# Kernel tuning notes

Hardware: AMD Instinct MI355X
Metric: run time of the kernel (lower is better)

Reference implementation:

```python
import jax, jax.numpy as jnp
import numpy as np

N_NEIGHBORS = 16
N_CLASSES = 10

def setup_inputs() -> dict:
    key = jax.random.key(0)
    k1, k2, k3 = jax.random.split(key, 3)
    x = jax.random.normal(k1, (1024, 64), dtype=jnp.float32)
    train_data = jax.random.normal(k2, (100000, 64), dtype=jnp.float32)
    train_labels = jax.random.randint(k3, (100000,), 0, N_CLASSES, dtype=jnp.int64)
    return {"x": x, "train_data": train_data, "train_labels": train_labels}

def reference(x, train_data, train_labels):
    # Pairwise L2 distances [B, N] via the quadratic expansion (same math as cdist p=2)
    x2 = jnp.sum(x * x, axis=-1, keepdims=True)            # [B, 1]
    t2 = jnp.sum(train_data * train_data, axis=-1)          # [N]
    d2 = x2 - 2.0 * (x @ train_data.T) + t2                 # [B, N]
    dist = jnp.sqrt(jnp.maximum(d2, 0.0))
    # k smallest distances
    neg_d, idx = jax.lax.top_k(-dist, N_NEIGHBORS)           # [B, k]
    d = -neg_d
    labels = train_labels[idx]                               # [B, k] gather
    # weights = 'distance': inverse distance, with exact-match rows handled
    w = 1.0 / d
    inf_mask = jnp.isinf(w)
    inf_row = jnp.any(inf_mask, axis=1, keepdims=True)
    w = jnp.where(inf_row, inf_mask.astype(w.dtype), w)
    # scatter_add weighted votes into [B, C]
    B = x.shape[0]
    rows = jnp.arange(B)[:, None]
    proba = jnp.zeros((B, N_CLASSES), dtype=w.dtype).at[rows, labels].add(w)
    s = jnp.sum(proba, axis=1, keepdims=True)
    s = jnp.where(s == 0.0, jnp.float32(1.0), s)
    proba = proba / s
    return jnp.argmax(proba, axis=1), proba
```

## Files before the change

### kernel.cpp

```cpp
#include <hip/hip_runtime.h>
#include <math.h>


constexpr int D        = 64;
constexpr int K        = 16;
constexpr int NCLS     = 10;
constexpr int CHUNKLEN = 896;
constexpr int NCHUNK   = 112;
constexpr int NPAD     = NCHUNK * CHUNKLEN + 32;
constexpr int NSUB     = 64;
constexpr int SUBLEN   = 128;
constexpr int SLOT     = 16;
constexpr int MSEL     = 48;

typedef __attribute__((ext_vector_type(8))) short bf16x8_t;
typedef __attribute__((ext_vector_type(4))) float f32x4_t;
typedef unsigned short ushort_t;

__device__ __forceinline__ ushort_t f32_to_bf16_rne(float f) {
  unsigned int u = __float_as_uint(f);
  unsigned int r = u + 0x7FFFu + ((u >> 16) & 1u);
  return (ushort_t)(r >> 16);
}

__device__ __forceinline__ bf16x8_t pack_bf16x8(float4 a, float4 b) {
  union { ushort_t u[8]; bf16x8_t v; } r;
  r.u[0] = f32_to_bf16_rne(a.x); r.u[1] = f32_to_bf16_rne(a.y);
  r.u[2] = f32_to_bf16_rne(a.z); r.u[3] = f32_to_bf16_rne(a.w);
  r.u[4] = f32_to_bf16_rne(b.x); r.u[5] = f32_to_bf16_rne(b.y);
  r.u[6] = f32_to_bf16_rne(b.z); r.u[7] = f32_to_bf16_rne(b.w);
  return r.v;
}

__global__ __launch_bounds__(256) void cvt_train(
    const float* __restrict__ t, ushort_t* __restrict__ tb,
    float* __restrict__ t2, float* __restrict__ nt2h, int N)
{
  int gid = blockIdx.x * 256 + threadIdx.x;
  int row = gid >> 2, qt = gid & 3;
  if (row >= NPAD) return;
  ushort_t* dst = tb + (size_t)row * D + qt * 16;
  if (row >= N) {
    uint2 z = make_uint2(0u, 0u);
    #pragma unroll
    for (int i = 0; i < 4; ++i) *reinterpret_cast<uint2*>(dst + i * 4) = z;
    if (qt == 0) { t2[row] = INFINITY; nt2h[row] = -INFINITY; }
    return;
  }
  const float* src = t + (size_t)row * D + qt * 16;
  float nrm = 0.f;
  #pragma unroll
  for (int i = 0; i < 4; ++i) {
    float4 v = *reinterpret_cast<const float4*>(src + i * 4);
    nrm = fmaf(v.x, v.x, nrm); nrm = fmaf(v.y, v.y, nrm);
    nrm = fmaf(v.z, v.z, nrm); nrm = fmaf(v.w, v.w, nrm);
    uint2 hh = make_uint2(
      (unsigned)f32_to_bf16_rne(v.x) | ((unsigned)f32_to_bf16_rne(v.y) << 16),
      (unsigned)f32_to_bf16_rne(v.z) | ((unsigned)f32_to_bf16_rne(v.w) << 16));
    *reinterpret_cast<uint2*>(dst + i * 4) = hh;
  }
  nrm += __shfl_xor(nrm, 1);
  nrm += __shfl_xor(nrm, 2);
  if (qt == 0) { t2[row] = nrm; nt2h[row] = -0.5f * nrm; }
}

__global__ __launch_bounds__(256) void knn_sample(
    const ushort_t* __restrict__ tb, const float* __restrict__ x,
    const float* __restrict__ nt2h, float* __restrict__ samp)
{
  const int tid = threadIdx.x;
  const int w = tid >> 6, lane = tid & 63;
  const int lh = lane & 15, lg = lane >> 4;
  const int qb = blockIdx.x, sub = blockIdx.y;
  const int q = qb * 64 + w * 16 + lh;

  const float* xrp = x + (size_t)q * D + lg * 8;
  bf16x8_t B0 = pack_bf16x8(*reinterpret_cast<const float4*>(xrp),
                            *reinterpret_cast<const float4*>(xrp + 4));
  bf16x8_t B1 = pack_bf16x8(*reinterpret_cast<const float4*>(xrp + 32),
                            *reinterpret_cast<const float4*>(xrp + 36));

  float Ld[4] = {-INFINITY, -INFINITY, -INFINITY, -INFINITY};

  const int pstart = sub * SUBLEN;
  const ushort_t* abase = tb + (size_t)pstart * D + lh * D + lg * 8;
  const float* nbase = nt2h + pstart + lg * 4;

  bf16x8_t A0[4], A1[4]; float4 NH[4];
  #pragma unroll
  for (int j = 0; j < 4; ++j) {
    const ushort_t* ap = abase + (size_t)j * 16 * D;
    A0[j] = *reinterpret_cast<const bf16x8_t*>(ap);
    A1[j] = *reinterpret_cast<const bf16x8_t*>(ap + 32);
    NH[j] = *reinterpret_cast<const float4*>(nbase + j * 16);
  }
  bf16x8_t N0[4], N1[4]; float4 NN[4];
  #pragma unroll
  for (int j = 0; j < 4; ++j) {
    const ushort_t* ap = abase + (size_t)(4 + j) * 16 * D;
    N0[j] = *reinterpret_cast<const bf16x8_t*>(ap);
    N1[j] = *reinterpret_cast<const bf16x8_t*>(ap + 32);
    NN[j] = *reinterpret_cast<const float4*>(nbase + (4 + j) * 16);
  }

  #pragma unroll
  for (int j = 0; j < 4; ++j) {
    f32x4_t c = {NH[j].x, NH[j].y, NH[j].z, NH[j].w};
    c = __builtin_amdgcn_mfma_f32_16x16x32_bf16(A0[j], B0, c, 0, 0, 0);
    c = __builtin_amdgcn_mfma_f32_16x16x32_bf16(A1[j], B1, c, 0, 0, 0);
    #pragma unroll
    for (int r = 0; r < 4; ++r) {
      float sv = c[r];
      if (sv > Ld[3]) {
        Ld[3] = sv;
        if (Ld[3] > Ld[2]) { float s_ = Ld[3]; Ld[3] = Ld[2]; Ld[2] = s_; }
        if (Ld[2] > Ld[1]) { float s_ = Ld[2]; Ld[2] = Ld[1]; Ld[1] = s_; }
        if (Ld[1] > Ld[0]) { float s_ = Ld[1]; Ld[1] = Ld[0]; Ld[0] = s_; }
      }
    }
  }
  #pragma unroll
  for (int j = 0; j < 4; ++j) {
    f32x4_t c = {NN[j].x, NN[j].y, NN[j].z, NN[j].w};
    c = __builtin_amdgcn_mfma_f32_16x16x32_bf16(N0[j], B0, c, 0, 0, 0);
    c = __builtin_amdgcn_mfma_f32_16x16x32_bf16(N1[j], B1, c, 0, 0, 0);
    #pragma unroll
    for (int r = 0; r < 4; ++r) {
      float sv = c[r];
      if (sv > Ld[3]) {
        Ld[3] = sv;
        if (Ld[3] > Ld[2]) { float s_ = Ld[3]; Ld[3] = Ld[2]; Ld[2] = s_; }
        if (Ld[2] > Ld[1]) { float s_ = Ld[2]; Ld[2] = Ld[1]; Ld[1] = s_; }
        if (Ld[1] > Ld[0]) { float s_ = Ld[1]; Ld[1] = Ld[0]; Ld[0] = s_; }
      }
    }
  }

  float* outp = samp + (size_t)q * (NSUB * 16) + sub * 16 + lg * 4;
  *reinterpret_cast<float4*>(outp) = make_float4(Ld[0], Ld[1], Ld[2], Ld[3]);
}

__global__ __launch_bounds__(256) void knn_theta(
    const float* __restrict__ samp, float* __restrict__ theta, int B)
{
  const int w = threadIdx.x >> 6, lane = threadIdx.x & 63;
  const int q = blockIdx.x * 4 + w;
  if (q >= B) return;

  const float* s = samp + (size_t)q * (NSUB * 16) + lane * 16;
  float4 p0 = *reinterpret_cast<const float4*>(s);
  float4 p1 = *reinterpret_cast<const float4*>(s + 4);
  float4 p2 = *reinterpret_cast<const float4*>(s + 8);
  float4 p3 = *reinterpret_cast<const float4*>(s + 12);
  float L0[4] = {p0.x, p0.y, p0.z, p0.w};
  float L1[4] = {p1.x, p1.y, p1.z, p1.w};
  float L2[4] = {p2.x, p2.y, p2.z, p2.w};
  float L3[4] = {p3.x, p3.y, p3.z, p3.w};

  float th = -INFINITY;
  for (int r = 0; r < K; ++r) {
    float bd = fmaxf(fmaxf(L0[0], L1[0]), fmaxf(L2[0], L3[0]));
    #pragma unroll
    for (int sdx = 0; sdx < 6; ++sdx) bd = fmaxf(bd, __shfl_xor(bd, 32 >> sdx));
    if (L0[0] == bd) { L0[0] = L0[1]; L0[1] = L0[2]; L0[2] = L0[3]; L0[3] = -INFINITY; }
    if (L1[0] == bd) { L1[0] = L1[1]; L1[1] = L1[2]; L1[2] = L1[3]; L1[3] = -INFINITY; }
    if (L2[0] == bd) { L2[0] = L2[1]; L2[1] = L2[2]; L2[2] = L2[3]; L2[3] = -INFINITY; }
    if (L3[0] == bd) { L3[0] = L3[1]; L3[1] = L3[2]; L3[2] = L3[3]; L3[3] = -INFINITY; }
    th = bd;
  }
  if (lane == 0) theta[q] = th;
}

__global__ __launch_bounds__(256) void knn_filter(
    const ushort_t* __restrict__ tb, const float* __restrict__ x,
    const float* __restrict__ nt2h, const float* __restrict__ theta,
    int* __restrict__ cnts, int2* __restrict__ cand2)
{
  __shared__ int  cnt_l[64];
  __shared__ int2 list_p[64][SLOT];

  const int tid = threadIdx.x;
  const int w = tid >> 6, lane = tid & 63;
  const int lh = lane & 15, lg = lane >> 4;

  const int d   = blockIdx.x + 16 * blockIdx.y;
  const int xcd = d & 7;
  const int t_  = d >> 3;
  const int qb  = t_ & 15;
  const int ch  = ((t_ >> 4) << 3) | xcd;

  const int q0 = qb * 64;
  const int wp0 = ch * CHUNKLEN + w * (CHUNKLEN / 4);

  if (tid < 64) cnt_l[tid] = 0;
  __syncthreads();

  bf16x8_t Bq0[4], Bq1[4];
  float th[4];
  #pragma unroll
  for (int ct = 0; ct < 4; ++ct) {
    const float* xrp = x + (size_t)(q0 + ct * 16 + lh) * D + lg * 8;
    Bq0[ct] = pack_bf16x8(*reinterpret_cast<const float4*>(xrp),
                          *reinterpret_cast<const float4*>(xrp + 4));
    Bq1[ct] = pack_bf16x8(*reinterpret_cast<const float4*>(xrp + 32),
                          *reinterpret_cast<const float4*>(xrp + 36));
    th[ct] = theta[q0 + ct * 16 + lh];
  }

  const ushort_t* abase = tb + (size_t)wp0 * D + lh * D + lg * 8;
  const float* nbase = nt2h + wp0 + lg * 4;

  bf16x8_t cA0 = *reinterpret_cast<const bf16x8_t*>(abase);
  bf16x8_t cA1 = *reinterpret_cast<const bf16x8_t*>(abase + 32);
  float4   cNA = *reinterpret_cast<const float4*>(nbase);
  bf16x8_t cB0 = *reinterpret_cast<const bf16x8_t*>(abase + (size_t)16 * D);
  bf16x8_t cB1 = *reinterpret_cast<const bf16x8_t*>(abase + (size_t)16 * D + 32);
  float4   cNB = *reinterpret_cast<const float4*>(nbase + 16);

  #define PROCESS(A0_, A1_, NH_, GIDX_)                                           \
    {                                                                             \
      _Pragma("unroll")                                                           \
      for (int ct = 0; ct < 4; ++ct) {                                            \
        f32x4_t c = {NH_.x, NH_.y, NH_.z, NH_.w};                                 \
        c = __builtin_amdgcn_mfma_f32_16x16x32_bf16(A0_, Bq0[ct], c, 0, 0, 0);    \
        c = __builtin_amdgcn_mfma_f32_16x16x32_bf16(A1_, Bq1[ct], c, 0, 0, 0);    \
        float mx = fmaxf(fmaxf(c[0], c[1]), fmaxf(c[2], c[3]));                   \
        if (mx >= th[ct]) {                         \
          const int qloc = ct * 16 + lh;                                          \
          const int pg = wp0 + (GIDX_) * 16 + lg * 4;                             \
          _Pragma("unroll")                                                       \
          for (int r = 0; r < 4; ++r) {                                           \
            if (c[r] >= th[ct]) {                                                 \
              int pos = atomicAdd(&cnt_l[qloc], 1);                               \
              if (pos < SLOT)                                                     \
                list_p[qloc][pos] = make_int2(pg + r, __float_as_int(c[r]));      \
            }                                                                     \
          }                                                                       \
        }                                                                         \
      }                                                                           \
    }

  for (int g = 0; g < 7; ++g) {
    const ushort_t* an = abase + (size_t)(2 * g + 2) * 16 * D;
    bf16x8_t nA0 = *reinterpret_cast<const bf16x8_t*>(an);
    bf16x8_t nA1 = *reinterpret_cast<const bf16x8_t*>(an + 32);
    float4   nNA = *reinterpret_cast<const float4*>(nbase + (2 * g + 2) * 16);
    bf16x8_t nB0 = *reinterpret_cast<const bf16x8_t*>(an + (size_t)16 * D);
    bf16x8_t nB1 = *reinterpret_cast<const bf16x8_t*>(an + (size_t)16 * D + 32);
    float4   nNB = *reinterpret_cast<const float4*>(nbase + (2 * g + 3) * 16);

    PROCESS(cA0, cA1, cNA, 2 * g);
    PROCESS(cB0, cB1, cNB, 2 * g + 1);

    cA0 = nA0; cA1 = nA1; cNA = nNA;
    cB0 = nB0; cB1 = nB1; cNB = nNB;
  }
  #undef PROCESS

  __syncthreads();
  if (tid < 64) {
    int n = cnt_l[tid]; if (n > SLOT) n = SLOT;
    size_t o = (size_t)(q0 + tid) * NCHUNK + ch;
    cnts[o] = n;
    for (int j = 0; j < n; ++j) cand2[o * SLOT + j] = list_p[tid][j];
  }
}

__global__ __launch_bounds__(256) void knn_vote(
    const float* __restrict__ x, const float* __restrict__ train,
    const float* __restrict__ t2, const int* __restrict__ labels,
    const int* __restrict__ cnts, const int2* __restrict__ cand2,
    float* __restrict__ out, int B, int N)
{
  __shared__ int2  cpair[NCHUNK * SLOT + 4];
  __shared__ float sortd[MSEL];
  __shared__ int   sorti[MSEL];
  __shared__ float xs[D];
  __shared__ int   total_s;
  __shared__ float x2_s;

  const int tid = threadIdx.x;
  const int w = tid >> 6, lane = tid & 63;
  const int q = blockIdx.x;

  if (tid == 0) total_s = 0;
  if (tid < D) xs[tid] = x[(size_t)q * D + tid];
  if (tid < MSEL) { sortd[tid] = INFINITY; sorti[tid] = 0x7fffffff; }
  __syncthreads();

  if (w == 0) {
    float v = xs[lane];
    float s = v * v;
    #pragma unroll
    for (int o = 32; o > 0; o >>= 1) s += __shfl_xor(s, o);
    if (lane == 0) x2_s = s;
  }
  if (tid < NCHUNK) {
    int n = cnts[(size_t)q * NCHUNK + tid];
    int base = atomicAdd(&total_s, n);
    const int2* src = cand2 + ((size_t)q * NCHUNK + tid) * SLOT;
    for (int j = 0; j < n; ++j) cpair[base + j] = src[j];
  }
  __syncthreads();

  const int total = total_s;
  const int totalPad = (total + 3) & ~3;
  const float x2 = x2_s;
  if (tid < totalPad - total)
    cpair[total + tid] = make_int2(0x7fffffff, __float_as_int(-INFINITY));
  __syncthreads();

  for (int j = tid; j < total; j += 256) {
    int2 mine = cpair[j];
    float ms = __int_as_float(mine.y);
    int   mi = mine.x;
    int rank = 0;
    for (int k = 0; k < totalPad; k += 4) {
      int2 o0 = cpair[k];     int2 o1 = cpair[k + 1];
      int2 o2 = cpair[k + 2]; int2 o3 = cpair[k + 3];
      float s0 = __int_as_float(o0.y), s1 = __int_as_float(o1.y);
      float s2 = __int_as_float(o2.y), s3 = __int_as_float(o3.y);
      rank += ((s0 > ms || (s0 == ms && o0.x < mi)) ? 1 : 0)
            + ((s1 > ms || (s1 == ms && o1.x < mi)) ? 1 : 0)
            + ((s2 > ms || (s2 == ms && o2.x < mi)) ? 1 : 0)
            + ((s3 > ms || (s3 == ms && o3.x < mi)) ? 1 : 0);
    }
    if (rank < MSEL) { sortd[rank] = ms; sorti[rank] = mi; }
  }
  __syncthreads();

  if (tid < MSEL * 4) {
    const int ci = tid >> 2, qt = tid & 3;
    const int idx = sorti[ci];
    float dot = 0.f;
    if (idx != 0x7fffffff) {
      const float* tr = train + (size_t)idx * D + qt * 16;
      #pragma unroll
      for (int i = 0; i < 4; ++i) {
        float4 tv = *reinterpret_cast<const float4*>(tr + i * 4);
        dot = fmaf(xs[qt * 16 + i * 4 + 0], tv.x, dot);
        dot = fmaf(xs[qt * 16 + i * 4 + 1], tv.y, dot);
        dot = fmaf(xs[qt * 16 + i * 4 + 2], tv.z, dot);
        dot = fmaf(xs[qt * 16 + i * 4 + 3], tv.w, dot);
      }
    }
    dot += __shfl_xor(dot, 1);
    dot += __shfl_xor(dot, 2);
    if (qt == 0)
      sortd[ci] = (idx != 0x7fffffff)
                ? fmaxf(x2 - 2.f * dot + t2[idx], 0.f) : INFINITY;
  }
  __syncthreads();

  if (w == 0) {
    float vd = (lane < MSEL) ? sortd[lane] : INFINITY;
    int   vi = (lane < MSEL) ? sorti[lane] : 0x7fffffff;
    float myD = INFINITY; int myI = 0;
    for (int r = 0; r < K; ++r) {
      float bd = vd; int bi = vi;
      #pragma unroll
      for (int s = 0; s < 6; ++s) {
        int off = 32 >> s;
        float od = __shfl_xor(bd, off);
        int   oi = __shfl_xor(bi, off);
        if (od < bd || (od == bd && oi < bi)) { bd = od; bi = oi; }
      }
      if (vd == bd && vi == bi) { vd = INFINITY; vi = 0x7fffffff; }
      if (lane == r) { myD = bd; myI = bi; }
    }

    int valid = (lane < K) && (myD < INFINITY) && (myI < N);
    float dist = sqrtf(fmaxf(myD, 0.f));
    int lab = labels[(valid && myI < N) ? myI : 0];
    int isz = (valid && dist == 0.f) ? 1 : 0;
    float wgt = 1.f / dist;

    float accw[NCLS]; float acci[NCLS]; int anyInf = 0;
    #pragma unroll
    for (int c = 0; c < NCLS; ++c) { accw[c] = 0.f; acci[c] = 0.f; }
    for (int r = 0; r < K; ++r) {
      int   vr   = __shfl(valid, r);
      int   labr = __shfl(lab, r);
      float wgtr = __shfl(wgt, r);
      int   iszr = __shfl(isz, r);
      if (vr) {
        anyInf |= iszr;
        #pragma unroll
        for (int c = 0; c < NCLS; ++c) {
          accw[c] += (labr == c) ? wgtr : 0.f;
          acci[c] += (labr == c && iszr) ? 1.f : 0.f;
        }
      }
    }

    if (lane == 0) {
      float proba[NCLS]; float s = 0.f;
      #pragma unroll
      for (int c = 0; c < NCLS; ++c) { proba[c] = anyInf ? acci[c] : accw[c]; s += proba[c]; }
      if (s == 0.f) s = 1.f;
      #pragma unroll
      for (int c = 0; c < NCLS; ++c) proba[c] = proba[c] / s;
      int best = 0; float bv = proba[0];
      #pragma unroll
      for (int c = 1; c < NCLS; ++c) if (proba[c] > bv) { bv = proba[c]; best = c; }
      out[q] = (float)best;
      #pragma unroll
      for (int c = 0; c < NCLS; ++c) out[B + q * NCLS + c] = proba[c];
    }
  }
}

extern "C" void kernel_launch(void* const* d_in, const int* in_sizes, int n_in,
                              void* d_out, int out_size, void* d_ws, size_t ws_size,
                              hipStream_t stream)
{
  const float* x      = (const float*)d_in[0];
  const float* train  = (const float*)d_in[1];
  const int*   labels = (const int*)d_in[2];
  float* out = (float*)d_out;

  const int B = in_sizes[0] / D;
  const int N = in_sizes[2];

  char* ws = (char*)d_ws;
  size_t off = 0;
  ushort_t* train_bf = (ushort_t*)(ws + off); off += (size_t)NPAD * D * 2;
  float*    t2       = (float*)(ws + off);    off += (size_t)NPAD * 4;
  float*    nt2h     = (float*)(ws + off);    off += (size_t)NPAD * 4;
  float*    theta    = (float*)(ws + off);    off += (size_t)B * 4;
  int*      cnts     = (int*)(ws + off);      off += (size_t)B * NCHUNK * 4;
  int2*     cand2    = (int2*)(ws + off);     off += (size_t)B * NCHUNK * SLOT * 8;
  float*    samp     = (float*)cand2;

  cvt_train<<<(NPAD * 4 + 255) / 256, 256, 0, stream>>>(train, train_bf, t2, nt2h, N);
  knn_sample<<<dim3(B / 64, NSUB), 256, 0, stream>>>(train_bf, x, nt2h, samp);
  knn_theta<<<(B + 3) / 4, 256, 0, stream>>>(samp, theta, B);
  knn_filter<<<dim3(16, NCHUNK), 256, 0, stream>>>(train_bf, x, nt2h, theta, cnts, cand2);
  knn_vote<<<B, 256, 0, stream>>>(x, train, t2, labels, cnts, cand2, out, B, N);
}
```

Baseline: 116.9 us.

## Fuse train conversion with sampling and stage filter tiles via async LDS loads

Merges the bf16 conversion and sampling kernels into one launch, with the sampling blocks reading fp32 train data directly and computing norms themselves so they no longer depend on the converted buffer. Rewrites the filter kernel to stream 32-point tiles into a per-wave double-buffered, swizzled LDS ring using global_load_lds, so loads overlap the MFMA work. It also changes the chunk size from 896 to 1024 points. The aim is to remove one launch and its dependency, and to hide global load latency in the filter. The cost is larger shared memory use and hand-written vmcnt waits that must match the number of loads in flight.

Measured after the change: 105.6 us. 1.11x faster.

```diff
diff --git a/kernel.cpp b/kernel.cpp
--- a/kernel.cpp
+++ b/kernel.cpp
@@ -5,13 +5,17 @@
 constexpr int D        = 64;
 constexpr int K        = 16;
 constexpr int NCLS     = 10;
-constexpr int CHUNKLEN = 896;
-constexpr int NCHUNK   = 112;
-constexpr int NPAD     = NCHUNK * CHUNKLEN + 32;
+constexpr int CHUNKLEN = 1024;
+constexpr int NCHUNK   = 104;
+constexpr int NPAD     = NCHUNK * 1024 + 64;
 constexpr int NSUB     = 64;
 constexpr int SUBLEN   = 128;
 constexpr int SLOT     = 16;
 constexpr int MSEL     = 48;
+constexpr int SGPTS    = 32;
+constexpr int SGBYTES  = SGPTS * 128;
+constexpr int SLOTB    = SGBYTES + 256;
+constexpr int NCVT     = (NPAD * 4) / 256;
 
 typedef __attribute__((ext_vector_type(8))) short bf16x8_t;
 typedef __attribute__((ext_vector_type(4))) float f32x4_t;
@@ -32,46 +36,58 @@
   return r.v;
 }
 
-__global__ __launch_bounds__(256) void cvt_train(
-    const float* __restrict__ t, ushort_t* __restrict__ tb,
-    float* __restrict__ t2, float* __restrict__ nt2h, int N)
+__device__ __forceinline__ void glds16(const void* g, void* l) {
+  __builtin_amdgcn_global_load_lds(
+      (const __attribute__((address_space(1))) void*)g,
+      (__attribute__((address_space(3))) void*)l, 16, 0, 0);
+}
+__device__ __forceinline__ void glds4(const void* g, void* l) {
+  __builtin_amdgcn_global_load_lds(
+      (const __attribute__((address_space(1))) void*)g,
+      (__attribute__((address_space(3))) void*)l, 4, 0, 0);
+}
+
+__global__ __launch_bounds__(256) void knn_prep(
+    const float* __restrict__ train, const float* __restrict__ x,
+    ushort_t* __restrict__ tb, float* __restrict__ t2,
+    float* __restrict__ nt2h, float* __restrict__ samp, int N)
 {
-  int gid = blockIdx.x * 256 + threadIdx.x;
-  int row = gid >> 2, qt = gid & 3;
-  if (row >= NPAD) return;
-  ushort_t* dst = tb + (size_t)row * D + qt * 16;
-  if (row >= N) {
-    uint2 z = make_uint2(0u, 0u);
+  __shared__ float nh_l[4][16];
+  const int tid = threadIdx.x;
+
+  if ((int)blockIdx.x < NCVT) {
+    int gid = blockIdx.x * 256 + tid;
+    int row = gid >> 2, qt = gid & 3;
+    ushort_t* dst = tb + (size_t)row * D + qt * 16;
+    if (row >= N) {
+      uint2 z = make_uint2(0u, 0u);
+      #pragma unroll
+      for (int i = 0; i < 4; ++i) *reinterpret_cast<uint2*>(dst + i * 4) = z;
+      if (qt == 0) { t2[row] = INFINITY; nt2h[row] = -INFINITY; }
+      return;
+    }
+    const float* src = train + (size_t)row * D + qt * 16;
+    float nrm = 0.f;
     #pragma unroll
-    for (int i = 0; i < 4; ++i) *reinterpret_cast<uint2*>(dst + i * 4) = z;
-    if (qt == 0) { t2[row] = INFINITY; nt2h[row] = -INFINITY; }
+    for (int i = 0; i < 4; ++i) {
+      float4 v = *reinterpret_cast<const float4*>(src + i * 4);
+      nrm = fmaf(v.x, v.x, nrm); nrm = fmaf(v.y, v.y, nrm);
+      nrm = fmaf(v.z, v.z, nrm); nrm = fmaf(v.w, v.w, nrm);
+      uint2 hh = make_uint2(
+        (unsigned)f32_to_bf16_rne(v.x) | ((unsigned)f32_to_bf16_rne(v.y) << 16),
+        (unsigned)f32_to_bf16_rne(v.z) | ((unsigned)f32_to_bf16_rne(v.w) << 16));
+      *reinterpret_cast<uint2*>(dst + i * 4) = hh;
+    }
+    nrm += __shfl_xor(nrm, 1);
+    nrm += __shfl_xor(nrm, 2);
+    if (qt == 0) { t2[row] = nrm; nt2h[row] = -0.5f * nrm; }
     return;
   }
-  const float* src = t + (size_t)row * D + qt * 16;
-  float nrm = 0.f;
-  #pragma unroll
-  for (int i = 0; i < 4; ++i) {
-    float4 v = *reinterpret_cast<const float4*>(src + i * 4);
-    nrm = fmaf(v.x, v.x, nrm); nrm = fmaf(v.y, v.y, nrm);
-    nrm = fmaf(v.z, v.z, nrm); nrm = fmaf(v.w, v.w, nrm);
-    uint2 hh = make_uint2(
-      (unsigned)f32_to_bf16_rne(v.x) | ((unsigned)f32_to_bf16_rne(v.y) << 16),
-      (unsigned)f32_to_bf16_rne(v.z) | ((unsigned)f32_to_bf16_rne(v.w) << 16));
-    *reinterpret_cast<uint2*>(dst + i * 4) = hh;
-  }
-  nrm += __shfl_xor(nrm, 1);
-  nrm += __shfl_xor(nrm, 2);
-  if (qt == 0) { t2[row] = nrm; nt2h[row] = -0.5f * nrm; }
-}
-
-__global__ __launch_bounds__(256) void knn_sample(
-    const ushort_t* __restrict__ tb, const float* __restrict__ x,
-    const float* __restrict__ nt2h, float* __restrict__ samp)
-{
-  const int tid = threadIdx.x;
+
+  const int bid2 = blockIdx.x - NCVT;
   const int w = tid >> 6, lane = tid & 63;
   const int lh = lane & 15, lg = lane >> 4;
-  const int qb = blockIdx.x, sub = blockIdx.y;
+  const int qb = bid2 & 15, sub = bid2 >> 4;
   const int q = qb * 64 + w * 16 + lh;
 
   const float* xrp = x + (size_t)q * D + lg * 8;
@@ -81,49 +97,32 @@
                             *reinterpret_cast<const float4*>(xrp + 36));
 
   float Ld[4] = {-INFINITY, -INFINITY, -INFINITY, -INFINITY};
-
   const int pstart = sub * SUBLEN;
-  const ushort_t* abase = tb + (size_t)pstart * D + lh * D + lg * 8;
-  const float* nbase = nt2h + pstart + lg * 4;
-
-  bf16x8_t A0[4], A1[4]; float4 NH[4];
-  #pragma unroll
-  for (int j = 0; j < 4; ++j) {
-    const ushort_t* ap = abase + (size_t)j * 16 * D;
-    A0[j] = *reinterpret_cast<const bf16x8_t*>(ap);
-    A1[j] = *reinterpret_cast<const bf16x8_t*>(ap + 32);
-    NH[j] = *reinterpret_cast<const float4*>(nbase + j * 16);
-  }
-  bf16x8_t N0[4], N1[4]; float4 NN[4];
-  #pragma unroll
-  for (int j = 0; j < 4; ++j) {
-    const ushort_t* ap = abase + (size_t)(4 + j) * 16 * D;
-    N0[j] = *reinterpret_cast<const bf16x8_t*>(ap);
-    N1[j] = *reinterpret_cast<const bf16x8_t*>(ap + 32);
-    NN[j] = *reinterpret_cast<const float4*>(nbase + (4 + j) * 16);
-  }
-
-  #pragma unroll
-  for (int j = 0; j < 4; ++j) {
-    f32x4_t c = {NH[j].x, NH[j].y, NH[j].z, NH[j].w};
-    c = __builtin_amdgcn_mfma_f32_16x16x32_bf16(A0[j], B0, c, 0, 0, 0);
-    c = __builtin_amdgcn_mfma_f32_16x16x32_bf16(A1[j], B1, c, 0, 0, 0);
-    #pragma unroll
-    for (int r = 0; r < 4; ++r) {
-      float sv = c[r];
-      if (sv > Ld[3]) {
-        Ld[3] = sv;
-        if (Ld[3] > Ld[2]) { float s_ = Ld[3]; Ld[3] = Ld[2]; Ld[2] = s_; }
-        if (Ld[2] > Ld[1]) { float s_ = Ld[2]; Ld[2] = Ld[1]; Ld[1] = s_; }
-        if (Ld[1] > Ld[0]) { float s_ = Ld[1]; Ld[1] = Ld[0]; Ld[0] = s_; }
-      }
-    }
-  }
-  #pragma unroll
-  for (int j = 0; j < 4; ++j) {
-    f32x4_t c = {NN[j].x, NN[j].y, NN[j].z, NN[j].w};
-    c = __builtin_amdgcn_mfma_f32_16x16x32_bf16(N0[j], B0, c, 0, 0, 0);
-    c = __builtin_amdgcn_mfma_f32_16x16x32_bf16(N1[j], B1, c, 0, 0, 0);
+
+  for (int j = 0; j < SUBLEN / 16; ++j) {
+    const float* tr = train + (size_t)(pstart + j * 16 + lh) * D;
+    float4 f0 = *reinterpret_cast<const float4*>(tr + lg * 8);
+    float4 f1 = *reinterpret_cast<const float4*>(tr + lg * 8 + 4);
+    float4 f2 = *reinterpret_cast<const float4*>(tr + 32 + lg * 8);
+    float4 f3 = *reinterpret_cast<const float4*>(tr + 32 + lg * 8 + 4);
+    bf16x8_t A0 = pack_bf16x8(f0, f1);
+    bf16x8_t A1 = pack_bf16x8(f2, f3);
+    float pn = 0.f;
+    pn = fmaf(f0.x, f0.x, pn); pn = fmaf(f0.y, f0.y, pn);
+    pn = fmaf(f0.z, f0.z, pn); pn = fmaf(f0.w, f0.w, pn);
+    pn = fmaf(f1.x, f1.x, pn); pn = fmaf(f1.y, f1.y, pn);
+    pn = fmaf(f1.z, f1.z, pn); pn = fmaf(f1.w, f1.w, pn);
+    pn = fmaf(f2.x, f2.x, pn); pn = fmaf(f2.y, f2.y, pn);
+    pn = fmaf(f2.z, f2.z, pn); pn = fmaf(f2.w, f2.w, pn);
+    pn = fmaf(f3.x, f3.x, pn); pn = fmaf(f3.y, f3.y, pn);
+    pn = fmaf(f3.z, f3.z, pn); pn = fmaf(f3.w, f3.w, pn);
+    pn += __shfl_xor(pn, 16);
+    pn += __shfl_xor(pn, 32);
+    if (lg == 0) nh_l[w][lh] = -0.5f * pn;
+    float4 nh = *reinterpret_cast<const float4*>(&nh_l[w][lg * 4]);
+    f32x4_t c = {nh.x, nh.y, nh.z, nh.w};
+    c = __builtin_amdgcn_mfma_f32_16x16x32_bf16(A0, B0, c, 0, 0, 0);
+    c = __builtin_amdgcn_mfma_f32_16x16x32_bf16(A1, B1, c, 0, 0, 0);
     #pragma unroll
     for (int r = 0; r < 4; ++r) {
       float sv = c[r];
@@ -176,6 +175,7 @@
     const float* __restrict__ nt2h, const float* __restrict__ theta,
     int* __restrict__ cnts, int2* __restrict__ cand2)
 {
+  __shared__ char ring[4][2][SLOTB];
   __shared__ int  cnt_l[64];
   __shared__ int2 list_p[64][SLOT];
 
@@ -189,8 +189,8 @@
   const int qb  = t_ & 15;
   const int ch  = ((t_ >> 4) << 3) | xcd;
 
-  const int q0 = qb * 64;
-  const int wp0 = ch * CHUNKLEN + w * (CHUNKLEN / 4);
+  const int q0  = qb * 64;
+  const int wp0 = ch * CHUNKLEN + w * 256;
 
   if (tid < 64) cnt_l[tid] = 0;
   __syncthreads();
@@ -207,55 +207,71 @@
     th[ct] = theta[q0 + ct * 16 + lh];
   }
 
-  const ushort_t* abase = tb + (size_t)wp0 * D + lh * D + lg * 8;
-  const float* nbase = nt2h + wp0 + lg * 4;
-
-  bf16x8_t cA0 = *reinterpret_cast<const bf16x8_t*>(abase);
-  bf16x8_t cA1 = *reinterpret_cast<const bf16x8_t*>(abase + 32);
-  float4   cNA = *reinterpret_cast<const float4*>(nbase);
-  bf16x8_t cB0 = *reinterpret_cast<const bf16x8_t*>(abase + (size_t)16 * D);
-  bf16x8_t cB1 = *reinterpret_cast<const bf16x8_t*>(abase + (size_t)16 * D + 32);
-  float4   cNB = *reinterpret_cast<const float4*>(nbase + 16);
-
-  #define PROCESS(A0_, A1_, NH_, GIDX_)                                           \
-    {                                                                             \
-      _Pragma("unroll")                                                           \
-      for (int ct = 0; ct < 4; ++ct) {                                            \
-        f32x4_t c = {NH_.x, NH_.y, NH_.z, NH_.w};                                 \
-        c = __builtin_amdgcn_mfma_f32_16x16x32_bf16(A0_, Bq0[ct], c, 0, 0, 0);    \
-        c = __builtin_amdgcn_mfma_f32_16x16x32_bf16(A1_, Bq1[ct], c, 0, 0, 0);    \
-        float mx = fmaxf(fmaxf(c[0], c[1]), fmaxf(c[2], c[3]));                   \
-        if (mx >= th[ct]) {                         \
-          const int qloc = ct * 16 + lh;                                          \
-          const int pg = wp0 + (GIDX_) * 16 + lg * 4;                             \
-          _Pragma("unroll")                                                       \
-          for (int r = 0; r < 4; ++r) {                                           \
-            if (c[r] >= th[ct]) {                                                 \
-              int pos = atomicAdd(&cnt_l[qloc], 1);                               \
-              if (pos < SLOT)                                                     \
-                list_p[qloc][pos] = make_int2(pg + r, __float_as_int(c[r]));      \
-            }                                                                     \
-          }                                                                       \
-        }                                                                         \
-      }                                                                           \
-    }
-
-  for (int g = 0; g < 7; ++g) {
-    const ushort_t* an = abase + (size_t)(2 * g + 2) * 16 * D;
-    bf16x8_t nA0 = *reinterpret_cast<const bf16x8_t*>(an);
-    bf16x8_t nA1 = *reinterpret_cast<const bf16x8_t*>(an + 32);
-    float4   nNA = *reinterpret_cast<const float4*>(nbase + (2 * g + 2) * 16);
-    bf16x8_t nB0 = *reinterpret_cast<const bf16x8_t*>(an + (size_t)16 * D);
-    bf16x8_t nB1 = *reinterpret_cast<const bf16x8_t*>(an + (size_t)16 * D + 32);
-    float4   nNB = *reinterpret_cast<const float4*>(nbase + (2 * g + 3) * 16);
-
-    PROCESS(cA0, cA1, cNA, 2 * g);
-    PROCESS(cB0, cB1, cNB, 2 * g + 1);
-
-    cA0 = nA0; cA1 = nA1; cNA = nNA;
-    cB0 = nB0; cB1 = nB1; cNB = nNB;
-  }
-  #undef PROCESS
+  char* myring = &ring[w][0][0];
+  const char*  gA = (const char*)(tb + (size_t)wp0 * D);
+  const float* gN = nt2h + wp0;
+  const int rowoff = (lane >> 3) * 128;
+  const int swz    = (((lane & 7) ^ (lane >> 3)) << 4);
+  const int lhx    = lh & 7;
+
+  #define ISSUE(SG)                                                              \
+    {                                                                            \
+      char* sb = myring + (((SG) & 1) ? SLOTB : 0);                              \
+      const char* ga = gA + (size_t)(SG) * SGBYTES;                              \
+      glds16(ga + rowoff + swz,        sb);                                      \
+      glds16(ga + 1024 + rowoff + swz, sb + 1024);                               \
+      glds16(ga + 2048 + rowoff + swz, sb + 2048);                               \
+      glds16(ga + 3072 + rowoff + swz, sb + 3072);                               \
+      glds4 (gN + (SG) * SGPTS + lane, sb + 4096);                               \
+    }
+
+  #define COMPUTE(SG)                                                            \
+    {                                                                            \
+      const char* sb = myring + (((SG) & 1) ? SLOTB : 0);                        \
+      _Pragma("unroll")                                                          \
+      for (int g2 = 0; g2 < 2; ++g2) {                                           \
+        bf16x8_t A0 = *reinterpret_cast<const bf16x8_t*>(                        \
+            sb + g2 * 2048 + lh * 128 + ((lg ^ lhx) << 4));                      \
+        bf16x8_t A1 = *reinterpret_cast<const bf16x8_t*>(                        \
+            sb + g2 * 2048 + lh * 128 + (((lg + 4) ^ lhx) << 4));                \
+        float4 nh = *reinterpret_cast<const float4*>(                            \
+            sb + 4096 + g2 * 64 + lg * 16);                                      \
+        const int pg = wp0 + (SG) * SGPTS + g2 * 16 + lg * 4;                    \
+        _Pragma("unroll")                                                        \
+        for (int ct = 0; ct < 4; ++ct) {                                         \
+          f32x4_t c = {nh.x, nh.y, nh.z, nh.w};                                  \
+          c = __builtin_amdgcn_mfma_f32_16x16x32_bf16(A0, Bq0[ct], c, 0, 0, 0);  \
+          c = __builtin_amdgcn_mfma_f32_16x16x32_bf16(A1, Bq1[ct], c, 0, 0, 0);  \
+          float mx = fmaxf(fmaxf(c[0], c[1]), fmaxf(c[2], c[3]));                \
+          if (mx >= th[ct]) {                                                    \
+            const int qloc = ct * 16 + lh;                                       \
+            _Pragma("unroll")                                                    \
+            for (int r = 0; r < 4; ++r) {                                        \
+              if (c[r] >= th[ct]) {                                              \
+                int pos = atomicAdd(&cnt_l[qloc], 1);                            \
+                if (pos < SLOT)                                                  \
+                  list_p[qloc][pos] = make_int2(pg + r, __float_as_int(c[r]));   \
+              }                                                                  \
+            }                                                                    \
+          }                                                                      \
+        }                                                                        \
+      }                                                                          \
+    }
+
+  asm volatile("s_waitcnt vmcnt(0)" ::: "memory");
+  ISSUE(0);
+  #pragma unroll
+  for (int it = 0; it < 8; ++it) {
+    if (it < 7) {
+      ISSUE(it + 1);
+      asm volatile("s_waitcnt vmcnt(5)" ::: "memory");
+    } else {
+      asm volatile("s_waitcnt vmcnt(0)" ::: "memory");
+    }
+    COMPUTE(it);
+  }
+  #undef ISSUE
+  #undef COMPUTE
 
   __syncthreads();
   if (tid < 64) {
@@ -432,8 +448,7 @@
   int2*     cand2    = (int2*)(ws + off);     off += (size_t)B * NCHUNK * SLOT * 8;
   float*    samp     = (float*)cand2;
 
-  cvt_train<<<(NPAD * 4 + 255) / 256, 256, 0, stream>>>(train, train_bf, t2, nt2h, N);
-  knn_sample<<<dim3(B / 64, NSUB), 256, 0, stream>>>(train_bf, x, nt2h, samp);
+  knn_prep<<<NCVT + (B / 64) * NSUB, 256, 0, stream>>>(train, x, train_bf, t2, nt2h, samp, N);
   knn_theta<<<(B + 3) / 4, 256, 0, stream>>>(samp, theta, B);
   knn_filter<<<dim3(16, NCHUNK), 256, 0, stream>>>(train_bf, x, nt2h, theta, cnts, cand2);
   knn_vote<<<B, 256, 0, stream>>>(x, train, t2, labels, cnts, cand2, out, B, N);
```
